# Kernel optimization log

Measured on AMD Instinct MI355X. Metric: run time of the kernel, lower is better.

Reference implementation:

```python
import math
import jax, jax.numpy as jnp
import numpy as np

B, S, D = 2, 2048, 3584
H, KVH, HD = 28, 4, 128
ROPE_THETA = 1000000.0

def setup_inputs() -> dict:
    key = jax.random.key(0)
    k1, k2, k3, k4, k5 = jax.random.split(key, 5)
    s = 0.02
    return {
        'hidden_states': jax.random.normal(k1, (B, S, D), jnp.float32),
        'Wq': jax.random.normal(k2, (D, H * HD), jnp.float32) * s,
        'Wk': jax.random.normal(k3, (D, KVH * HD), jnp.float32) * s,
        'Wv': jax.random.normal(k4, (D, KVH * HD), jnp.float32) * s,
        'Wo': jax.random.normal(k5, (H * HD, D), jnp.float32) * s,
    }

def _rotate_half(x):
    x1, x2 = x[..., :x.shape[-1] // 2], x[..., x.shape[-1] // 2:]
    return jnp.concatenate((-x2, x1), axis=-1)

def _rope_tables(seq_len, dim, base):
    inv_freq = 1.0 / base ** (jnp.arange(0, dim, 2, dtype=jnp.float32) / dim)
    t = jnp.arange(seq_len, dtype=jnp.float32)
    freqs = jnp.outer(t, inv_freq)  # [S, dim/2]
    emb = jnp.concatenate((freqs, freqs), axis=-1)  # [S, dim]
    return jnp.cos(emb), jnp.sin(emb)

def reference(hidden_states, Wq, Wk, Wv, Wo):
    b, s, _ = hidden_states.shape
    q = (hidden_states @ Wq).reshape(b, s, H, HD)
    k = (hidden_states @ Wk).reshape(b, s, KVH, HD)
    v = (hidden_states @ Wv).reshape(b, s, KVH, HD)

    cos, sin = _rope_tables(s, HD, ROPE_THETA)
    cos = cos.astype(q.dtype)[None, :, None, :]  # [1,S,1,HD]
    sin = sin.astype(q.dtype)[None, :, None, :]
    q = q * cos + _rotate_half(q) * sin
    k = k * cos + _rotate_half(k) * sin

    groups = H // KVH  # 7
    k = jnp.repeat(k, groups, axis=2)
    v = jnp.repeat(v, groups, axis=2)

    q = jnp.transpose(q, (0, 2, 1, 3))  # [B,H,S,HD]
    k = jnp.transpose(k, (0, 2, 1, 3))
    v = jnp.transpose(v, (0, 2, 1, 3))

    scale = 1.0 / math.sqrt(HD)
    scores = jnp.einsum('bhqd,bhkd->bhqk', q, k) * scale
    causal = jnp.tril(jnp.ones((s, s), dtype=bool))[None, None]
    scores = scores + jnp.where(causal, 0.0, -1e9).astype(scores.dtype)
    attn = jax.nn.softmax(scores, axis=-1)
    out = jnp.einsum('bhqk,bhkd->bhqd', attn, v)
    out = jnp.transpose(out, (0, 2, 1, 3)).reshape(b, s, H * HD)
    return out @ Wo
```

## Files before the change

kernel.cpp:

```cpp
#include <hip/hip_runtime.h>
#include <hip/hip_bf16.h>
#include <cstdint>

typedef __attribute__((ext_vector_type(8))) __bf16 bf16x8;
typedef __attribute__((ext_vector_type(4))) float f32x4;
typedef unsigned short u16;

#define B_    2
#define S_    2048
#define D_    3584
#define H_    28
#define KVH_  4
#define HD_   128
#define GQA_  7
#define QKVN  4608
#define QK2SCALE 0.12751744416014806f

#define WAITV(N) asm volatile("s_waitcnt vmcnt(" #N ")" ::: "memory")
#define WAITL(N) asm volatile("s_waitcnt lgkmcnt(" #N ")" ::: "memory")

__device__ __forceinline__ u16 f2bf(float f){
  union { float f; uint32_t u; } v; v.f = f;
  uint32_t u = v.u + 0x7fffu + ((v.u >> 16) & 1u);
  return (u16)(u >> 16);
}
__device__ __forceinline__ float bf2f(u16 h){
  union { uint32_t u; float f; } v; v.u = ((uint32_t)h) << 16; return v.f;
}
__device__ __forceinline__ float exp2a(float x){
  float r; asm("v_exp_f32 %0, %1" : "=v"(r) : "v"(x)); return r;
}
__device__ __forceinline__ uint32_t cvtpk(float lo, float hi){
  uint32_t r; asm("v_cvt_pk_bf16_f32 %0, %1, %2" : "=v"(r) : "v"(lo), "v"(hi)); return r;
}

typedef void __attribute__((address_space(1))) as1void;
typedef void __attribute__((address_space(3))) as3void;
__device__ __forceinline__ void gload16(const void* g, void* l){
  __builtin_amdgcn_global_load_lds((as1void*)g, (as3void*)l, 16, 0, 0);
}

__global__ __launch_bounds__(256) void convx_kernel(const float* __restrict__ in, u16* __restrict__ outp, int n4){
  int i = blockIdx.x*256 + threadIdx.x;
  if (i < n4){
    float4 v = ((const float4*)in)[i];
    ushort4 o; o.x=f2bf(v.x); o.y=f2bf(v.y); o.z=f2bf(v.z); o.w=f2bf(v.w);
    ((ushort4*)outp)[i] = o;
  }
}

__global__ __launch_bounds__(256) void tconv_kernel(const float* __restrict__ in, u16* __restrict__ outp, int R, int C){
  __shared__ float t[32][33];
  int r = threadIdx.x >> 5, c = threadIdx.x & 31;
  int r0 = blockIdx.y*32, c0 = blockIdx.x*32;
  #pragma unroll
  for (int i=0;i<4;i++) t[r+8*i][c] = in[(size_t)(r0 + r + 8*i)*C + c0 + c];
  __syncthreads();
  #pragma unroll
  for (int i=0;i<4;i++) outp[(size_t)(c0 + r + 8*i)*R + r0 + c] = f2bf(t[c][r+8*i]);
}

__global__ __launch_bounds__(256) void tbf16_kernel(const u16* __restrict__ in, u16* __restrict__ outp, int R, int C, int instride){
  const u16* inb = in + (size_t)blockIdx.z*R*instride;
  u16* outb = outp + (size_t)blockIdx.z*R*C;
  __shared__ u16 t[32][33];
  int r = threadIdx.x >> 5, c = threadIdx.x & 31;
  int r0 = blockIdx.y*32, c0 = blockIdx.x*32;
  #pragma unroll
  for (int i=0;i<4;i++) t[r+8*i][c] = inb[(size_t)(r0+r+8*i)*instride + c0+c];
  __syncthreads();
  #pragma unroll
  for (int i=0;i<4;i++) outb[(size_t)(c0+r+8*i)*R + r0+c] = t[c][r+8*i];
}

__global__ __launch_bounds__(256) void ropetab_kernel(float* __restrict__ cost, float* __restrict__ sint){
  int i = blockIdx.x*256 + threadIdx.x;
  int s = i >> 6, d = i & 63;
  float inv = powf(1.0e6f, -(float)d * (1.0f/64.0f));
  float a = (float)s * inv;
  cost[i] = cosf(a); sint[i] = sinf(a);
}

__global__ __launch_bounds__(256) void rope_kernel(u16* __restrict__ x, const float* __restrict__ cost,
                                                   const float* __restrict__ sint){
  int i = blockIdx.x*256 + threadIdx.x;
  int d = i & 63;
  int h = (i >> 6) & 31;
  int bs = i >> 11;
  int s = bs & (S_-1);
  float sc = (h < H_) ? QK2SCALE : 1.0f;
  size_t base = (size_t)bs*QKVN + (size_t)h*128 + d;
  float x0 = bf2f(x[base]), x1 = bf2f(x[base+64]);
  float cv = cost[s*64+d], sv = sint[s*64+d];
  x[base]    = f2bf((x0*cv - x1*sv)*sc);
  x[base+64] = f2bf((x1*cv + x0*sv)*sc);
}

__global__ __launch_bounds__(256) void gemm128_kernel(const u16* __restrict__ A, const u16* __restrict__ Bt,
                                                      u16* __restrict__ C, int M, int N, int K, int ldc, int coloff){
  __shared__ u16 As[128*32];
  __shared__ u16 Bs[128*32];
  const int tid = threadIdx.x;
  const int l = tid & 63, lg = l >> 4, lm = l & 15;
  const int w = tid >> 6, wr = w >> 1, wc = w & 1;
  const int m0 = blockIdx.y * 128, n0 = blockIdx.x * 128;

  f32x4 acc[4][4];
  #pragma unroll
  for (int m=0;m<4;++m)
    #pragma unroll
    for (int n=0;n<4;++n) acc[m][n] = (f32x4){0.f,0.f,0.f,0.f};

  const int nkt = K >> 5;
  for (int kt = 0; kt < nkt; ++kt){
    __syncthreads();
    const int kb = kt*32;
    #pragma unroll
    for (int j = 0; j < 2; ++j){
      int g = j*256 + tid;
      int row = g >> 2, wi = g & 3;
      int ksrc = kb + ((wi ^ (row & 3)) << 3);
      gload16(A  + (size_t)(m0+row)*K + ksrc, (char*)As + j*4096 + (tid & 192)*16);
      gload16(Bt + (size_t)(n0+row)*K + ksrc, (char*)Bs + j*4096 + (tid & 192)*16);
    }
    __syncthreads();
    bf16x8 af[4], bfr[4];
    #pragma unroll
    for (int m = 0; m < 4; ++m){
      int r = wr*64 + m*16 + lm;
      af[m] = *(const bf16x8*)((const char*)As + r*64 + (lg ^ (r & 3))*16);
    }
    #pragma unroll
    for (int n = 0; n < 4; ++n){
      int r = wc*64 + n*16 + lm;
      bfr[n] = *(const bf16x8*)((const char*)Bs + r*64 + (lg ^ (r & 3))*16);
    }
    #pragma unroll
    for (int m = 0; m < 4; ++m)
      #pragma unroll
      for (int n = 0; n < 4; ++n)
        acc[m][n] = __builtin_amdgcn_mfma_f32_16x16x32_bf16(af[m], bfr[n], acc[m][n], 0,0,0);
  }
  #pragma unroll
  for (int m=0;m<4;++m)
    #pragma unroll
    for (int n=0;n<4;++n)
      #pragma unroll
      for (int r=0;r<4;++r){
        int row = m0 + wr*64 + m*16 + lg*4 + r;
        int col = coloff + n0 + wc*64 + n*16 + lm;
        C[(size_t)row*ldc + col] = f2bf(acc[m][n][r]);
      }
}

template<bool OUTF32>
__global__ __launch_bounds__(512) void gemm256_kernel(const u16* __restrict__ A, const u16* __restrict__ Bt,
                                                      void* __restrict__ Cv, int M, int N, int K, int nbx,
                                                      int ldc, int coloff){
  extern __shared__ char lds[];
  const int tid = threadIdx.x;
  const int l = tid & 63, lg = l >> 4, lm = l & 15;
  const int w = tid >> 6, wr = w >> 2, wc = w & 3;
  const int srow = tid >> 3, swi = tid & 7;

  const int nwg = (int)gridDim.x;
  const int q8 = nwg >> 3, r8 = nwg & 7;
  const int xcd = blockIdx.x & 7, pos = blockIdx.x >> 3;
  const int wg = (xcd < r8 ? xcd*(q8+1) : r8*(q8+1) + (xcd - r8)*q8) + pos;
  const int m0 = (wg / nbx) * 256, n0 = (wg % nbx) * 256;

  f32x4 acc[8][4];
  #pragma unroll
  for (int m=0;m<8;++m)
    #pragma unroll
    for (int n=0;n<4;++n) acc[m][n] = (f32x4){0.f,0.f,0.f,0.f};
  bf16x8 aF[8][2], bF[4][2];

  auto stage = [&](int T, int ht){
    const u16* p = (ht < 2) ? (A + (size_t)(m0 + (ht << 7))*K)
                            : (Bt + (size_t)(n0 + ((ht - 2) << 7))*K);
    char* d = lds + ((size_t)(T & 1) << 16) + (ht << 14) + ((tid & 448) << 4);
    #pragma unroll
    for (int j = 0; j < 2; ++j){
      int r = (j << 6) + srow;
      gload16(p + (size_t)r*K + (size_t)T*64 + ((swi ^ (r & 7)) << 3), d + (j << 13));
    }
  };
  auto ldA = [&](int c, int mh){
    const char* base = lds + (c << 16) + (wr << 14);
    #pragma unroll
    for (int m = 0; m < 4; ++m){
      int r = ((mh*4 + m) << 4) + lm;
      #pragma unroll
      for (int kk = 0; kk < 2; ++kk)
        aF[mh*4+m][kk] = *(const bf16x8*)(base + r*128 + (((kk*4 + lg) ^ (r & 7)) << 4));
    }
  };
  auto ldB = [&](int c, int nh){
    #pragma unroll
    for (int n = 0; n < 2; ++n){
      int rb = wc*64 + ((nh*2 + n) << 4) + lm;
      const char* base = lds + (c << 16) + 32768 + ((rb >> 7) << 14);
      int ri = rb & 127;
      #pragma unroll
      for (int kk = 0; kk < 2; ++kk)
        bF[nh*2+n][kk] = *(const bf16x8*)(base + ri*128 + (((kk*4 + lg) ^ (ri & 7)) << 4));
    }
  };
  auto mmaQ = [&](int mh, int nh){
    __builtin_amdgcn_s_setprio(1);
    #pragma unroll
    for (int m = 0; m < 4; ++m)
      #pragma unroll
      for (int n = 0; n < 2; ++n)
        #pragma unroll
        for (int kk = 0; kk < 2; ++kk)
          acc[mh*4+m][nh*2+n] = __builtin_amdgcn_mfma_f32_16x16x32_bf16(
              aF[mh*4+m][kk], bF[nh*2+n][kk], acc[mh*4+m][nh*2+n], 0,0,0);
    __builtin_amdgcn_s_setprio(0);
  };

  const int nkt = K >> 6;
  stage(0,0); stage(0,1); stage(0,2); stage(0,3);
  stage(1,2); stage(1,0); stage(1,1);
  WAITV(6);
  __builtin_amdgcn_s_barrier();

  for (int t = 0; t < nkt; ++t){
    const int c = t & 1;
    ldA(c,0); ldB(c,0); ldB(c,1);
    if (t + 1 < nkt) stage(t+1, 3);
    WAITL(4);
    __builtin_amdgcn_s_barrier();
    mmaQ(0,0);
    WAITL(0);
    __builtin_amdgcn_s_barrier();
    ldA(c,1);
    if (t + 2 < nkt) stage(t+2, 2);
    __builtin_amdgcn_s_barrier();
    mmaQ(0,1);
    WAITL(0);
    __builtin_amdgcn_s_barrier();
    if (t + 2 < nkt) stage(t+2, 0);
    __builtin_amdgcn_s_barrier();
    mmaQ(1,0);
    __builtin_amdgcn_s_barrier();
    if (t + 2 < nkt){ stage(t+2, 1); WAITV(6); }
    else if (t + 1 < nkt){ WAITV(0); }
    __builtin_amdgcn_s_barrier();
    mmaQ(1,1);
    __builtin_amdgcn_s_barrier();
  }

  #pragma unroll
  for (int m = 0; m < 8; ++m)
    #pragma unroll
    for (int n = 0; n < 4; ++n)
      #pragma unroll
      for (int r = 0; r < 4; ++r){
        int row = m0 + wr*128 + m*16 + lg*4 + r;
        int col = coloff + n0 + wc*64 + n*16 + lm;
        if (OUTF32) ((float*)Cv)[(size_t)row*ldc + col] = acc[m][n][r];
        else        ((u16*)Cv)[(size_t)row*ldc + col] = f2bf(acc[m][n][r]);
      }
}

__global__ __launch_bounds__(512, 4) void attn_kernel(const u16* __restrict__ QKV, const u16* __restrict__ Vt,
                                                      u16* __restrict__ O){
  __shared__ u16 Kl[2][8192];
  __shared__ u16 Vl[8192];
  const int id = blockIdx.x;
  const int qt = (S_/128 - 1) - id/(H_*B_);
  const int hb = id % (H_*B_);
  const int h = hb % H_, b = hb / H_;
  const int kvh = h / GQA_;
  const int tid = threadIdx.x;
  const int w = tid >> 6, l = tid & 63, lg = l >> 4, lm = l & 15;

  const int qrowA = qt*128 + w*16 + lm;
  const u16* qptr = QKV + (size_t)(b*S_ + qrowA)*QKVN + h*HD_;
  bf16x8 qf[4];
  #pragma unroll
  for (int ks = 0; ks < 4; ++ks) qf[ks] = *(const bf16x8*)(qptr + ks*32 + lg*8);
  WAITV(0);
  asm volatile("" :: "v"(qf[0]), "v"(qf[1]), "v"(qf[2]), "v"(qf[3]));

  const int qrowD = qt*128 + w*16 + lg*4;
  float m_run[4], l_run[4];
  f32x4 oacc[8];
  #pragma unroll
  for (int r=0;r<4;++r){ m_run[r] = -3.0e38f; l_run[r] = 0.0f; }
  #pragma unroll
  for (int dn=0;dn<8;++dn) oacc[dn] = (f32x4){0.f,0.f,0.f,0.f};

  const u16* Kbase = QKV + (size_t)(b*S_)*QKVN + H_*HD_ + kvh*HD_;
  const u16* Vbase = Vt + (size_t)(b*KVH_ + kvh)*HD_*S_;

  auto stageK = [&](int bufi, int ktv){
    const int kb = ktv*64;
    #pragma unroll
    for (int j = 0; j < 2; ++j){
      int g = j*512 + tid;
      int kp = g >> 4, wik = g & 15;
      gload16(Kbase + (size_t)(kb + kp)*QKVN + (wik ^ (kp & 7))*8,
              (char*)Kl + bufi*16384 + j*8192 + (tid & 448)*16);
    }
  };
  auto stageV = [&](int ktv){
    const int kb = ktv*64;
    #pragma unroll
    for (int j = 0; j < 2; ++j){
      int g = j*512 + tid;
      int dd = g >> 3, wiv = g & 7;
      gload16(Vbase + (size_t)dd*S_ + kb + (wiv ^ (dd & 7))*8,
              (char*)Vl + j*8192 + (tid & 448)*16);
    }
  };

  const int nkt = 2*qt + 2;
  int cur = 0;
  stageK(0, 0); stageV(0); stageK(1, 1);
  for (int kt = 0; kt < nkt; ++kt){
    if (kt + 1 < nkt){ WAITV(2); }
    else             { WAITV(0); }
    __builtin_amdgcn_s_barrier();
    const int cb = cur*16384;

    f32x4 sf[4];
    __builtin_amdgcn_s_setprio(1);
    #pragma unroll
    for (int n = 0; n < 4; ++n){
      sf[n] = (f32x4){0.f,0.f,0.f,0.f};
      int kp = n*16 + lm;
      #pragma unroll
      for (int ks = 0; ks < 4; ++ks){
        bf16x8 kf = *(const bf16x8*)((const char*)Kl + cb + kp*256 + (((ks*4 + lg) ^ (kp & 7))*16));
        sf[n] = __builtin_amdgcn_mfma_f32_16x16x32_bf16(qf[ks], kf, sf[n], 0,0,0);
      }
    }
    __builtin_amdgcn_s_setprio(0);

    const bool tmask = (kt >= 2*qt);
    float p[4][4], rmax[4];
    #pragma unroll
    for (int r=0;r<4;++r) rmax[r] = -3.0e38f;
    #pragma unroll
    for (int n=0;n<4;++n)
      #pragma unroll
      for (int r=0;r<4;++r){
        float v = sf[n][r];
        if (tmask && (kt*64 + n*16 + lm) > (qrowD + r)) v -= 1.0e9f;
        p[n][r] = v;
        rmax[r] = fmaxf(rmax[r], v);
      }
    #pragma unroll
    for (int o_=1; o_<16; o_<<=1)
      #pragma unroll
      for (int r=0;r<4;++r) rmax[r] = fmaxf(rmax[r], __shfl_xor(rmax[r], o_, 64));

    bool grow = (rmax[0] > m_run[0]) | (rmax[1] > m_run[1]) | (rmax[2] > m_run[2]) | (rmax[3] > m_run[3]);
    if (__any(grow)){
      #pragma unroll
      for (int r=0;r<4;++r){
        float mn = fmaxf(m_run[r], rmax[r]);
        float corr = exp2a(m_run[r] - mn);
        m_run[r] = mn;
        l_run[r] *= corr;
        #pragma unroll
        for (int dn=0;dn<8;++dn) oacc[dn][r] *= corr;
      }
    }
    #pragma unroll
    for (int n=0;n<4;++n)
      #pragma unroll
      for (int r=0;r<4;++r){ p[n][r] = exp2a(p[n][r] - m_run[r]); l_run[r] += p[n][r]; }

    __builtin_amdgcn_s_barrier();
    char* Pl = (char*)Kl + cb;
    #pragma unroll
    for (int n=0;n<4;++n)
      #pragma unroll
      for (int rp=0;rp<2;++rp){
        uint32_t pk = cvtpk(p[n][2*rp], p[n][2*rp+1]);
        int q0 = w*16 + lg*4 + 2*rp;
        int kp = n*16 + lm;
        *(u16*)(Pl + q0*128     + ((kp >> 3) ^ (q0 & 7))*16       + (kp & 7)*2) = (u16)pk;
        *(u16*)(Pl + (q0+1)*128 + ((kp >> 3) ^ ((q0+1) & 7))*16   + (kp & 7)*2) = (u16)(pk >> 16);
      }

    __builtin_amdgcn_s_setprio(1);
    #pragma unroll
    for (int ks=0; ks<2; ++ks){
      int q_ = w*16 + lm;
      bf16x8 pf = *(const bf16x8*)(Pl + q_*128 + (((ks*4 + lg) ^ (q_ & 7))*16));
      #pragma unroll
      for (int dn=0;dn<8;++dn){
        int dd = dn*16 + lm;
        bf16x8 vf = *(const bf16x8*)((const char*)Vl + dd*128 + (((ks*4 + lg) ^ (dd & 7))*16));
        oacc[dn] = __builtin_amdgcn_mfma_f32_16x16x32_bf16(pf, vf, oacc[dn], 0,0,0);
      }
    }
    __builtin_amdgcn_s_setprio(0);

    WAITL(0);
    __builtin_amdgcn_s_barrier();
    if (kt + 1 < nkt) stageV(kt+1);
    if (kt + 2 < nkt) stageK(cur, kt+2);
    cur ^= 1;
  }

  #pragma unroll
  for (int o_=1; o_<16; o_<<=1)
    #pragma unroll
    for (int r=0;r<4;++r) l_run[r] += __shfl_xor(l_run[r], o_, 64);

  float inv_l[4];
  #pragma unroll
  for (int r=0;r<4;++r) inv_l[r] = 1.0f / l_run[r];
  #pragma unroll
  for (int dn=0;dn<8;++dn)
    #pragma unroll
    for (int r=0;r<4;++r)
      O[(size_t)(b*S_ + qrowD + r)*(H_*HD_) + h*HD_ + dn*16 + lm] = f2bf(oacc[dn][r]*inv_l[r]);
}

extern "C" void kernel_launch(void* const* d_in, const int* in_sizes, int n_in,
                              void* d_out, int out_size, void* d_ws, size_t ws_size,
                              hipStream_t stream) {
  const float* X  = (const float*)d_in[0];
  const float* Wq = (const float*)d_in[1];
  const float* Wk = (const float*)d_in[2];
  const float* Wv = (const float*)d_in[3];
  const float* Wo = (const float*)d_in[4];
  float* out = (float*)d_out;

  char* ws = (char*)d_ws;
  size_t off = 0;
  auto alloc = [&](size_t bytes)->void*{ void* p = ws + off; off += (bytes + 255) & ~(size_t)255; return p; };
  const size_t MB = (size_t)B_*S_;
  u16* Xb   = (u16*)alloc(MB*D_*2);
  u16* Wqkv = (u16*)alloc((size_t)D_*QKVN*2);
  u16* Wot  = (u16*)alloc((size_t)H_*HD_*D_*2);
  u16* QKVb = (u16*)alloc(MB*QKVN*2);
  float* cost = (float*)alloc((size_t)S_*64*4);
  float* sint = (float*)alloc((size_t)S_*64*4);
  u16* AO  = Xb;
  u16* Vtg = Wqkv;

  (void)hipFuncSetAttribute(reinterpret_cast<const void*>(gemm256_kernel<false>),
                            hipFuncAttributeMaxDynamicSharedMemorySize, 131072);
  (void)hipFuncSetAttribute(reinterpret_cast<const void*>(gemm256_kernel<true>),
                            hipFuncAttributeMaxDynamicSharedMemorySize, 131072);

  convx_kernel<<<dim3((MB*D_/4 + 255)/256), 256, 0, stream>>>(X, Xb, (int)(MB*D_/4));
  tconv_kernel<<<dim3(D_/32, D_/32), 256, 0, stream>>>(Wq, Wqkv, D_, H_*HD_);
  tconv_kernel<<<dim3((KVH_*HD_)/32, D_/32), 256, 0, stream>>>(Wk, Wqkv + (size_t)(H_*HD_)*D_, D_, KVH_*HD_);
  tconv_kernel<<<dim3((KVH_*HD_)/32, D_/32), 256, 0, stream>>>(Wv, Wqkv + (size_t)(H_*HD_ + KVH_*HD_)*D_, D_, KVH_*HD_);
  tconv_kernel<<<dim3(D_/32, (H_*HD_)/32), 256, 0, stream>>>(Wo, Wot, H_*HD_, D_);
  ropetab_kernel<<<dim3(S_*64/256), 256, 0, stream>>>(cost, sint);
  gemm256_kernel<false><<<dim3((D_/256)*(MB/256)), 512, 131072, stream>>>(Xb, Wqkv, QKVb, (int)MB, D_, D_, D_/256, QKVN, 0);
  gemm128_kernel<<<dim3((KVH_*HD_*2)/128, MB/128), 256, 0, stream>>>(Xb, Wqkv + (size_t)(H_*HD_)*D_, QKVb, (int)MB, KVH_*HD_*2, D_, QKVN, H_*HD_);
  rope_kernel<<<dim3(MB*32*64/256), 256, 0, stream>>>(QKVb, cost, sint);
  tbf16_kernel<<<dim3((KVH_*HD_)/32, S_/32, B_), 256, 0, stream>>>(QKVb + (H_+KVH_)*HD_, Vtg, S_, KVH_*HD_, QKVN);
  attn_kernel<<<dim3((S_/128)*H_*B_), 512, 0, stream>>>(QKVb, Vtg, AO);
  gemm256_kernel<true><<<dim3((D_/256)*(MB/256)), 512, 131072, stream>>>(AO, Wot, out, (int)MB, D_, H_*HD_, D_/256, D_, 0);
}
```

Baseline: 481.3 us.

## Transpose QK^T MFMA so each lane owns one query row in softmax

Swaps the MFMA operand order for the score computation so the accumulator is S^T, giving each lane all 16 key values of a single query row. Row max and row sum then need only two cross-lane shuffles instead of four per row, and the running max and sum become scalars per lane. P is written to LDS as packed 32-bit stores instead of 16-bit halves. The correction factors and the final normalisation are redistributed to the output layout with __shfl, which adds a few shuffles in exchange for the cheaper reductions.

Result: faster. 461.6 us (-4.1%).

```diff
diff --git a/kernel.cpp b/kernel.cpp
--- a/kernel.cpp
+++ b/kernel.cpp
@@ -285,11 +285,10 @@
   WAITV(0);
   asm volatile("" :: "v"(qf[0]), "v"(qf[1]), "v"(qf[2]), "v"(qf[3]));
 
+  const int qcol  = qrowA;
   const int qrowD = qt*128 + w*16 + lg*4;
-  float m_run[4], l_run[4];
+  float m_run = -3.0e38f, l_run = 0.0f;
   f32x4 oacc[8];
-  #pragma unroll
-  for (int r=0;r<4;++r){ m_run[r] = -3.0e38f; l_run[r] = 0.0f; }
   #pragma unroll
   for (int dn=0;dn<8;++dn) oacc[dn] = (f32x4){0.f,0.f,0.f,0.f};
 
@@ -335,58 +334,59 @@
       #pragma unroll
       for (int ks = 0; ks < 4; ++ks){
         bf16x8 kf = *(const bf16x8*)((const char*)Kl + cb + kp*256 + (((ks*4 + lg) ^ (kp & 7))*16));
-        sf[n] = __builtin_amdgcn_mfma_f32_16x16x32_bf16(qf[ks], kf, sf[n], 0,0,0);
+        sf[n] = __builtin_amdgcn_mfma_f32_16x16x32_bf16(kf, qf[ks], sf[n], 0,0,0);
       }
     }
     __builtin_amdgcn_s_setprio(0);
 
     const bool tmask = (kt >= 2*qt);
-    float p[4][4], rmax[4];
-    #pragma unroll
-    for (int r=0;r<4;++r) rmax[r] = -3.0e38f;
+    float p[4][4];
+    float rmax = -3.0e38f;
     #pragma unroll
     for (int n=0;n<4;++n)
       #pragma unroll
       for (int r=0;r<4;++r){
         float v = sf[n][r];
-        if (tmask && (kt*64 + n*16 + lm) > (qrowD + r)) v -= 1.0e9f;
+        if (tmask && (kt*64 + n*16 + lg*4 + r) > qcol) v -= 1.0e9f;
         p[n][r] = v;
-        rmax[r] = fmaxf(rmax[r], v);
+        rmax = fmaxf(rmax, v);
       }
-    #pragma unroll
-    for (int o_=1; o_<16; o_<<=1)
-      #pragma unroll
-      for (int r=0;r<4;++r) rmax[r] = fmaxf(rmax[r], __shfl_xor(rmax[r], o_, 64));
-
-    bool grow = (rmax[0] > m_run[0]) | (rmax[1] > m_run[1]) | (rmax[2] > m_run[2]) | (rmax[3] > m_run[3]);
-    if (__any(grow)){
-      #pragma unroll
-      for (int r=0;r<4;++r){
-        float mn = fmaxf(m_run[r], rmax[r]);
-        float corr = exp2a(m_run[r] - mn);
-        m_run[r] = mn;
-        l_run[r] *= corr;
+    rmax = fmaxf(rmax, __shfl_xor(rmax, 16, 64));
+    rmax = fmaxf(rmax, __shfl_xor(rmax, 32, 64));
+
+    if (__any(rmax > m_run)){
+      float mn = fmaxf(m_run, rmax);
+      float corr = exp2a(m_run - mn);
+      m_run = mn;
+      l_run *= corr;
+      float corr_r[4];
+      #pragma unroll
+      for (int r=0;r<4;++r) corr_r[r] = __shfl(corr, lg*4 + r, 64);
+      #pragma unroll
+      for (int dn=0;dn<8;++dn)
         #pragma unroll
-        for (int dn=0;dn<8;++dn) oacc[dn][r] *= corr;
-      }
-    }
+        for (int r=0;r<4;++r) oacc[dn][r] *= corr_r[r];
+    }
+    float psum = 0.f;
     #pragma unroll
     for (int n=0;n<4;++n)
       #pragma unroll
-      for (int r=0;r<4;++r){ p[n][r] = exp2a(p[n][r] - m_run[r]); l_run[r] += p[n][r]; }
+      for (int r=0;r<4;++r){ p[n][r] = exp2a(p[n][r] - m_run); psum += p[n][r]; }
+    l_run += psum;
 
     __builtin_amdgcn_s_barrier();
     char* Pl = (char*)Kl + cb;
-    #pragma unroll
-    for (int n=0;n<4;++n)
-      #pragma unroll
-      for (int rp=0;rp<2;++rp){
-        uint32_t pk = cvtpk(p[n][2*rp], p[n][2*rp+1]);
-        int q0 = w*16 + lg*4 + 2*rp;
-        int kp = n*16 + lm;
-        *(u16*)(Pl + q0*128     + ((kp >> 3) ^ (q0 & 7))*16       + (kp & 7)*2) = (u16)pk;
-        *(u16*)(Pl + (q0+1)*128 + ((kp >> 3) ^ ((q0+1) & 7))*16   + (kp & 7)*2) = (u16)(pk >> 16);
-      }
+    {
+      int q_ = w*16 + lm;
+      #pragma unroll
+      for (int n=0;n<4;++n)
+        #pragma unroll
+        for (int j=0;j<2;++j){
+          uint32_t pk = cvtpk(p[n][2*j], p[n][2*j+1]);
+          int kp = n*16 + lg*4 + 2*j;
+          *(uint32_t*)(Pl + q_*128 + (((kp >> 3) ^ (q_ & 7))*16) + (kp & 7)*2) = pk;
+        }
+    }
 
     __builtin_amdgcn_s_setprio(1);
     #pragma unroll
@@ -409,19 +409,17 @@
     cur ^= 1;
   }
 
-  #pragma unroll
-  for (int o_=1; o_<16; o_<<=1)
-    #pragma unroll
-    for (int r=0;r<4;++r) l_run[r] += __shfl_xor(l_run[r], o_, 64);
-
-  float inv_l[4];
-  #pragma unroll
-  for (int r=0;r<4;++r) inv_l[r] = 1.0f / l_run[r];
+  l_run += __shfl_xor(l_run, 16, 64);
+  l_run += __shfl_xor(l_run, 32, 64);
+  float inv = 1.0f / l_run;
+  float inv_r[4];
+  #pragma unroll
+  for (int r=0;r<4;++r) inv_r[r] = __shfl(inv, lg*4 + r, 64);
   #pragma unroll
   for (int dn=0;dn<8;++dn)
     #pragma unroll
     for (int r=0;r<4;++r)
-      O[(size_t)(b*S_ + qrowD + r)*(H_*HD_) + h*HD_ + dn*16 + lm] = f2bf(oacc[dn][r]*inv_l[r]);
+      O[(size_t)(b*S_ + qrowD + r)*(H_*HD_) + h*HD_ + dn*16 + lm] = f2bf(oacc[dn][r]*inv_r[r]);
 }
 
 extern "C" void kernel_launch(void* const* d_in, const int* in_sizes, int n_in,
```
